# Performance work log

Measured on AMD Instinct MI355X. Metric: run time of the kernel, lower is better.

The kernel has to match this reference:

```python
import jax, jax.numpy as jnp
import numpy as np

N_NODES = 50000
N_EDGES = 1600000
NODE_DIM = 16
EDGE_DIM = 16
PIPE_F = 4
HID = 64
L = 3


def _lin(k, fan_in, fan_out):
    kw, kb = jax.random.split(k)
    bound = 1.0 / np.sqrt(fan_in)
    w = jax.random.uniform(kw, (fan_in, fan_out), jnp.float32, -bound, bound)
    b = jax.random.uniform(kb, (fan_out,), jnp.float32, -bound, bound)
    return w, b


def setup_inputs() -> dict:
    key = jax.random.key(0)
    ks = jax.random.split(key, 16)
    leak_area = jax.random.normal(ks[0], (N_NODES, 1), jnp.float32)
    pipe_attrs = jax.random.normal(ks[1], (N_EDGES, PIPE_F), jnp.float32)
    edge_index = jax.random.randint(ks[2], (2, N_EDGES), 0, N_NODES, jnp.int32)
    node_embed_w, node_embed_b = _lin(ks[3], 1, NODE_DIM)
    edge_embed_w, edge_embed_b = _lin(ks[4], PIPE_F, EDGE_DIM)
    # per-layer MLP params, stacked along leading layer axis
    ew1, eb1, ew2, eb2, nw1, nb1, nw2, nb2 = [], [], [], [], [], [], [], []
    for l in range(L):
        kl = jax.random.fold_in(ks[5], l)
        k1, k2, k3, k4 = jax.random.split(kl, 4)
        w, b = _lin(k1, 2 * NODE_DIM + EDGE_DIM, HID); ew1.append(w); eb1.append(b)
        w, b = _lin(k2, HID, EDGE_DIM); ew2.append(w); eb2.append(b)
        w, b = _lin(k3, NODE_DIM + EDGE_DIM, HID); nw1.append(w); nb1.append(b)
        w, b = _lin(k4, HID, NODE_DIM); nw2.append(w); nb2.append(b)
    final_node_w, final_node_b = _lin(ks[6], NODE_DIM, 1)
    final_edge_w, final_edge_b = _lin(ks[7], EDGE_DIM, 1)
    return {
        "leak_area": leak_area,
        "pipe_attrs": pipe_attrs,
        "edge_index": edge_index,
        "node_embed_w": node_embed_w, "node_embed_b": node_embed_b,
        "edge_embed_w": edge_embed_w, "edge_embed_b": edge_embed_b,
        "edge_mlp_w1": jnp.stack(ew1), "edge_mlp_b1": jnp.stack(eb1),
        "edge_mlp_w2": jnp.stack(ew2), "edge_mlp_b2": jnp.stack(eb2),
        "node_mlp_w1": jnp.stack(nw1), "node_mlp_b1": jnp.stack(nb1),
        "node_mlp_w2": jnp.stack(nw2), "node_mlp_b2": jnp.stack(nb2),
        "final_node_w": final_node_w, "final_node_b": final_node_b,
        "final_edge_w": final_edge_w, "final_edge_b": final_edge_b,
    }


def reference(leak_area, pipe_attrs, edge_index,
              node_embed_w, node_embed_b, edge_embed_w, edge_embed_b,
              edge_mlp_w1, edge_mlp_b1, edge_mlp_w2, edge_mlp_b2,
              node_mlp_w1, node_mlp_b1, node_mlp_w2, node_mlp_b2,
              final_node_w, final_node_b, final_edge_w, final_edge_b):
    x = leak_area @ node_embed_w + node_embed_b          # [N, node_dim]
    e = pipe_attrs @ edge_embed_w + edge_embed_b          # [E, edge_dim]
    src = edge_index[0]  # x_j (source, PyG default flow source_to_target)
    dst = edge_index[1]  # x_i (target); aggregation index
    n = x.shape[0]
    num_layers = edge_mlp_w1.shape[0]
    ones = jnp.ones((src.shape[0], 1), x.dtype)
    deg = jax.ops.segment_sum(ones, dst, num_segments=n)  # [N,1]
    inv_deg = 1.0 / jnp.maximum(deg, 1.0)
    for l in range(num_layers):
        # message: small MLP on [x_i, x_j, e] per edge
        m_in = jnp.concatenate([x[dst], x[src], e], axis=-1)       # [E, 2d+de]
        h = jax.nn.relu(m_in @ edge_mlp_w1[l] + edge_mlp_b1[l])    # [E, 64]
        msg = h @ edge_mlp_w2[l] + edge_mlp_b2[l]                  # [E, de]
        # mean-aggregate to target nodes
        aggr = jax.ops.segment_sum(msg, dst, num_segments=n) * inv_deg  # [N, de]
        # node update MLP
        u_in = jnp.concatenate([x, aggr], axis=-1)                 # [N, d+de]
        x = jax.nn.relu(u_in @ node_mlp_w1[l] + node_mlp_b1[l]) @ node_mlp_w2[l] + node_mlp_b2[l]
    H = (x @ final_node_w + final_node_b)[:, 0]   # [N]
    q = (e @ final_edge_w + final_edge_b)[:, 0]   # [E]
    return H, q
```

## Files before the change

### kernel.cpp

```cpp
#include <hip/hip_runtime.h>
#include <hip/hip_bf16.h>

#define NN 50000
#define NE 1600000
#define NB 391
#define CBLK 392
#define EPB 4096

typedef __attribute__((ext_vector_type(8))) short bf16x8;
typedef __attribute__((ext_vector_type(4))) float f32x4;

#define B_HAG   0
#define B_QW    (B_HAG + NN*64*4)
#define B_NF    (B_QW + 32)
#define B_W1B   (B_NF + 3*8*64*8*2)
#define B_XB0   (B_W1B + 3*8*64*8*2)
#define B_XB1   (B_XB0 + NN*16*2)
#define B_EPK   (B_XB1 + NN*16*2)
#define B_OFF   (B_EPK + NE*16)
#define B_BCNT  (B_OFF + (NN+1)*4)
#define B_BASE  (B_BCNT + CBLK*NB*4)
#define B_GTOT  (B_BASE + (NB+1)*4)
#define B_END   (B_GTOT + NB*4)

static __device__ __forceinline__ unsigned short f2bf(float f) {
    union { __hip_bfloat16 h; unsigned short u; } cv;
    cv.h = __float2bfloat16(f);
    return cv.u;
}
static __device__ __forceinline__ unsigned pk2(float a, float b) {
    unsigned r;
    asm("v_cvt_pk_bf16_f32 %0, %1, %2" : "=v"(r) : "v"(a), "v"(b));
    return r;
}
static __device__ __forceinline__ float bf2f(unsigned short u) {
    return __uint_as_float((unsigned)u << 16);
}
static __device__ __forceinline__ bf16x8 mk8(unsigned a, unsigned b, unsigned c, unsigned d) {
    union { bf16x8 v; uint4 u; } cv;
    cv.u = make_uint4(a, b, c, d);
    return cv.v;
}

__global__ void prep_kernel(const float* __restrict__ ew1, const float* __restrict__ eb1,
                            const float* __restrict__ nw1, const float* __restrict__ ew2,
                            const float* __restrict__ nw2,
                            const float* __restrict__ eeW, const float* __restrict__ eeB,
                            const float* __restrict__ few, const float* __restrict__ feb,
                            unsigned short* __restrict__ w1b, unsigned short* __restrict__ nf,
                            float* __restrict__ qw)
{
    int t0 = blockIdx.x * blockDim.x + threadIdx.x;
    int stride = gridDim.x * blockDim.x;
    for (int idx = t0; idx < 3 * 8 * 64 * 8; idx += stride) {
        int l = idx >> 12;
        int r = idx & 4095;
        int f = r >> 9;
        int lane = (r >> 3) & 63;
        int e = r & 7;
        int col = lane & 15;
        int krow = ((lane >> 4) << 3) + e;
        {
            int tt = f >> 1, s = f & 1;
            int k = krow + (s << 5);
            int j = (tt << 4) + col;
            float v = 0.f;
            if (k < 32) {
                v = ew1[l * 3072 + k * 64 + j];
            } else if (k < 36) {
                int f2 = k - 32;
                float acc = 0.f;
                for (int m = 0; m < 16; m++) acc += eeW[f2 * 16 + m] * ew1[l * 3072 + (32 + m) * 64 + j];
                v = acc;
            } else if (k == 36) {
                float acc = eb1[l * 64 + j];
                for (int m = 0; m < 16; m++) acc += eeB[m] * ew1[l * 3072 + (32 + m) * 64 + j];
                v = acc;
            }
            w1b[idx] = f2bf(v);
        }
        {
            float v;
            if (f < 2)      v = ew2[l * 1024 + (f * 32 + krow) * 16 + col];
            else if (f < 6) v = nw1[l * 2048 + krow * 64 + (f - 2) * 16 + col];
            else            v = nw2[l * 1024 + ((f - 6) * 32 + krow) * 16 + col];
            nf[idx] = f2bf(v);
        }
    }
    if (t0 < 4) {
        float s = 0.f;
        for (int k = 0; k < 16; k++) s += eeW[t0 * 16 + k] * few[k];
        qw[t0] = s;
    } else if (t0 == 4) {
        float s = feb[0];
        for (int k = 0; k < 16; k++) s += eeB[k] * few[k];
        qw[4] = s;
    }
}

__global__ __launch_bounds__(256) void node_init_kernel(
    const float* __restrict__ leak, const float* __restrict__ nw, const float* __restrict__ nb,
    unsigned short* __restrict__ xb0, float* __restrict__ hag)
{
    int n = blockIdx.x * blockDim.x + threadIdx.x;
    if (n >= NN) return;
    float la = leak[n];
    float v[16];
    #pragma unroll
    for (int i = 0; i < 16; i++) v[i] = la * nw[i] + nb[i];
    unsigned pk[8];
    #pragma unroll
    for (int i = 0; i < 8; i++) pk[i] = pk2(v[2 * i], v[2 * i + 1]);
    uint4* xo = reinterpret_cast<uint4*>(xb0 + n * 16);
    xo[0] = make_uint4(pk[0], pk[1], pk[2], pk[3]);
    xo[1] = make_uint4(pk[4], pk[5], pk[6], pk[7]);
    float4 z = {0.f, 0.f, 0.f, 0.f};
    float4* hp = reinterpret_cast<float4*>(hag + n * 64);
    #pragma unroll
    for (int j = 0; j < 16; j++) hp[j] = z;
}

__global__ __launch_bounds__(1024) void bucket_count_kernel(
    const int* __restrict__ dst, int* __restrict__ bcnt)
{
    __shared__ int hist[NB];
    int t = threadIdx.x;
    for (int i = t; i < NB; i += 1024) hist[i] = 0;
    __syncthreads();
    int base = blockIdx.x * EPB;
    int b[4];
    #pragma unroll
    for (int i = 0; i < 4; i++) {
        int idx = base + i * 1024 + t;
        b[i] = (idx < NE) ? (dst[idx] >> 7) : -1;
    }
    #pragma unroll
    for (int i = 0; i < 4; i++)
        if (b[i] >= 0) atomicAdd(&hist[b[i]], 1);
    __syncthreads();
    for (int i = t; i < NB; i += 1024) bcnt[blockIdx.x * NB + i] = hist[i];
}

__global__ __launch_bounds__(512) void scan_blocks_kernel(
    int* __restrict__ bcnt, int* __restrict__ gtot)
{
    __shared__ int sm[512];
    int b = blockIdx.x;
    int t = threadIdx.x;
    int v = (t < CBLK) ? bcnt[t * NB + b] : 0;
    sm[t] = v;
    __syncthreads();
    for (int o = 1; o < 512; o <<= 1) {
        int x = (t >= o) ? sm[t - o] : 0;
        __syncthreads();
        sm[t] += x;
        __syncthreads();
    }
    if (t < CBLK) bcnt[t * NB + b] = sm[t] - v;
    if (t == 511) gtot[b] = sm[511];
}

__global__ __launch_bounds__(512) void scan_top_kernel(
    const int* __restrict__ gtot, int* __restrict__ gbase)
{
    __shared__ int sm[512];
    int t = threadIdx.x;
    int v = (t < NB) ? gtot[t] : 0;
    sm[t] = v;
    __syncthreads();
    for (int o = 1; o < 512; o <<= 1) {
        int x = (t >= o) ? sm[t - o] : 0;
        __syncthreads();
        sm[t] += x;
        __syncthreads();
    }
    if (t < NB) gbase[t] = sm[t] - v;
    if (t == 0) gbase[NB] = NE;
}

__global__ __launch_bounds__(1024) void bucket_scatter_kernel(
    const int* __restrict__ ei, const float* __restrict__ pa,
    const int* __restrict__ bcnt, const int* __restrict__ gbase,
    const float* __restrict__ qw,
    float* __restrict__ qout, uint4* __restrict__ epk)
{
    __shared__ int hist[NB];
    int t = threadIdx.x;
    for (int i = t; i < NB; i += 1024) hist[i] = 0;
    __syncthreads();
    int base = blockIdx.x * EPB;
    float q0 = qw[0], q1 = qw[1], q2 = qw[2], q3 = qw[3], q4 = qw[4];
    int d[4], s[4];
    float4 p[4];
    #pragma unroll
    for (int i = 0; i < 4; i++) {
        int idx = base + i * 1024 + t;
        if (idx < NE) {
            d[i] = ei[NE + idx];
            s[i] = ei[idx];
            p[i] = reinterpret_cast<const float4*>(pa)[idx];
        } else {
            d[i] = -1;
        }
    }
    #pragma unroll
    for (int i = 0; i < 4; i++) {
        int idx = base + i * 1024 + t;
        if (d[i] >= 0)
            qout[idx] = q4 + p[i].x * q0 + p[i].y * q1 + p[i].z * q2 + p[i].w * q3;
    }
    int lr[4];
    #pragma unroll
    for (int i = 0; i < 4; i++)
        if (d[i] >= 0) lr[i] = atomicAdd(&hist[d[i] >> 7], 1);
    int bs[4];
    #pragma unroll
    for (int i = 0; i < 4; i++)
        if (d[i] >= 0) {
            int b = d[i] >> 7;
            bs[i] = gbase[b] + bcnt[blockIdx.x * NB + b];
        }
    #pragma unroll
    for (int i = 0; i < 4; i++)
        if (d[i] >= 0) {
            uint4 v;
            v.x = (unsigned)s[i];
            v.y = (unsigned)d[i];
            v.z = pk2(p[i].x, p[i].y);
            v.w = pk2(p[i].z, p[i].w);
            epk[bs[i] + lr[i]] = v;
        }
}

__global__ __launch_bounds__(1024) void fine_sort_kernel(
    const int* __restrict__ gbase, uint4* __restrict__ epk, int* __restrict__ off)
{
    __shared__ int hist[128];
    __shared__ int fb[128];
    int t = threadIdx.x;
    int b = blockIdx.x;
    int S = gbase[b], E = gbase[b + 1];
    if (t < 128) hist[t] = 0;
    __syncthreads();

    uint4 r[12];
    #pragma unroll
    for (int i = 0; i < 12; i++) {
        int gi = S + i * 1024 + t;
        if (gi < E) r[i] = epk[gi];
    }
    int lr[12];
    #pragma unroll
    for (int i = 0; i < 12; i++) {
        int gi = S + i * 1024 + t;
        if (gi < E) lr[i] = atomicAdd(&hist[(int)(r[i].y & 127u)], 1);
    }
    __syncthreads();
    if (t < 128) fb[t] = hist[t];
    __syncthreads();
    for (int o = 1; o < 128; o <<= 1) {
        int v = 0;
        if (t < 128 && t >= o) v = fb[t - o];
        __syncthreads();
        if (t < 128) fb[t] += v;
        __syncthreads();
    }
    int d0 = b << 7;
    if (t < 128 && d0 + t < NN) off[d0 + t] = S + fb[t] - hist[t];
    if (b == NB - 1 && t == 0) off[NN] = NE;
    __syncthreads();
    #pragma unroll
    for (int i = 0; i < 12; i++) {
        int gi = S + i * 1024 + t;
        if (gi < E) {
            int fd = (int)(r[i].y & 127u);
            int pos = S + (fb[fd] - hist[fd]) + lr[i];
            epk[pos] = r[i];
        }
    }
}

__global__ __launch_bounds__(128, 5) void edge_mfma_kernel(
    const unsigned short* __restrict__ xb,
    const uint4* __restrict__ epk,
    const int* __restrict__ off,
    const unsigned short* __restrict__ w1b,
    float* __restrict__ hag)
{
    __shared__ unsigned short hbuf[2][64 * 68];
    int tid = threadIdx.x;
    int lane = tid & 63;
    int wid = tid >> 6;
    int wave = blockIdx.x * 2 + wid;
    int base = wave * 64;
    if (base >= NE) return;
    int ar = lane & 15;
    int ap = lane >> 4;
    unsigned short* hb = &hbuf[wid][0];

    uint4 ev0 = epk[base + 0  + ar];
    uint4 ev1 = epk[base + 16 + ar];
    uint4 ev2 = epk[base + 32 + ar];
    uint4 ev3 = epk[base + 48 + ar];

    int r0 = (ap < 2) ? (int)ev0.y : (int)ev0.x;
    int r1 = (ap < 2) ? (int)ev1.y : (int)ev1.x;
    int r2 = (ap < 2) ? (int)ev2.y : (int)ev2.x;
    int r3 = (ap < 2) ? (int)ev3.y : (int)ev3.x;
    int half = (ap & 1) * 8;
    bf16x8 a00 = *reinterpret_cast<const bf16x8*>(xb + (size_t)r0 * 16 + half);
    bf16x8 a01 = *reinterpret_cast<const bf16x8*>(xb + (size_t)r1 * 16 + half);
    bf16x8 a02 = *reinterpret_cast<const bf16x8*>(xb + (size_t)r2 * 16 + half);
    bf16x8 a03 = *reinterpret_cast<const bf16x8*>(xb + (size_t)r3 * 16 + half);

    int d0 = __builtin_amdgcn_readfirstlane((int)ev0.y);

    bf16x8 Bf[8];
    const bf16x8* w1v = reinterpret_cast<const bf16x8*>(w1b);
    #pragma unroll
    for (int i = 0; i < 8; i++) Bf[i] = w1v[i * 64 + lane];

#define DO_TILE(EV, A0, TILE) do {                                             \
    bf16x8 a1 = (bf16x8)0;                                                     \
    if (ap == 0) {                                                             \
        a1[0] = (short)(EV.z & 0xffffu);                                       \
        a1[1] = (short)(EV.z >> 16);                                           \
        a1[2] = (short)(EV.w & 0xffffu);                                       \
        a1[3] = (short)(EV.w >> 16);                                           \
        a1[4] = (short)0x3f80;                                                 \
    }                                                                          \
    f32x4 C0 = {0.f, 0.f, 0.f, 0.f}, C1 = C0, C2 = C0, C3 = C0;                \
    C0 = __builtin_amdgcn_mfma_f32_16x16x32_bf16(A0, Bf[0], C0, 0, 0, 0);      \
    C0 = __builtin_amdgcn_mfma_f32_16x16x32_bf16(a1, Bf[1], C0, 0, 0, 0);      \
    C1 = __builtin_amdgcn_mfma_f32_16x16x32_bf16(A0, Bf[2], C1, 0, 0, 0);      \
    C1 = __builtin_amdgcn_mfma_f32_16x16x32_bf16(a1, Bf[3], C1, 0, 0, 0);      \
    C2 = __builtin_amdgcn_mfma_f32_16x16x32_bf16(A0, Bf[4], C2, 0, 0, 0);      \
    C2 = __builtin_amdgcn_mfma_f32_16x16x32_bf16(a1, Bf[5], C2, 0, 0, 0);      \
    C3 = __builtin_amdgcn_mfma_f32_16x16x32_bf16(A0, Bf[6], C3, 0, 0, 0);      \
    C3 = __builtin_amdgcn_mfma_f32_16x16x32_bf16(a1, Bf[7], C3, 0, 0, 0);      \
    int eoff = TILE * 16 + ap * 4;                                             \
    {                                                                          \
        unsigned lov = pk2(fmaxf(C0[0], 0.f), fmaxf(C0[1], 0.f));              \
        unsigned hiv = pk2(fmaxf(C0[2], 0.f), fmaxf(C0[3], 0.f));              \
        *reinterpret_cast<uint2*>(hb + (0 * 16 + ar) * 68 + eoff) = make_uint2(lov, hiv); \
    }                                                                          \
    {                                                                          \
        unsigned lov = pk2(fmaxf(C1[0], 0.f), fmaxf(C1[1], 0.f));              \
        unsigned hiv = pk2(fmaxf(C1[2], 0.f), fmaxf(C1[3], 0.f));              \
        *reinterpret_cast<uint2*>(hb + (1 * 16 + ar) * 68 + eoff) = make_uint2(lov, hiv); \
    }                                                                          \
    {                                                                          \
        unsigned lov = pk2(fmaxf(C2[0], 0.f), fmaxf(C2[1], 0.f));              \
        unsigned hiv = pk2(fmaxf(C2[2], 0.f), fmaxf(C2[3], 0.f));              \
        *reinterpret_cast<uint2*>(hb + (2 * 16 + ar) * 68 + eoff) = make_uint2(lov, hiv); \
    }                                                                          \
    {                                                                          \
        unsigned lov = pk2(fmaxf(C3[0], 0.f), fmaxf(C3[1], 0.f));              \
        unsigned hiv = pk2(fmaxf(C3[2], 0.f), fmaxf(C3[3], 0.f));              \
        *reinterpret_cast<uint2*>(hb + (3 * 16 + ar) * 68 + eoff) = make_uint2(lov, hiv); \
    }                                                                          \
} while (0)

    DO_TILE(ev0, a00, 0);
    DO_TILE(ev1, a01, 1);
    DO_TILE(ev2, a02, 2);
    DO_TILE(ev3, a03, 3);
#undef DO_TILE

    asm volatile("s_waitcnt lgkmcnt(0)" ::: "memory");
    __builtin_amdgcn_sched_barrier(0);

    int d = d0;
    int e = base;
    const int lim = base + 64;
    const unsigned short* hr = hb + lane * 68;
    while (e < lim) {
        int segend = off[d + 1];
        int eend = segend < lim ? segend : lim;
        float acc = 0.f;
        int i = e - base, iend = eend - base;
        for (; (i & 3) != 0 && i < iend; ++i) acc += bf2f(hr[i]);
        for (; i + 4 <= iend; i += 4) {
            uint2 u = *reinterpret_cast<const uint2*>(hr + i);
            acc += __uint_as_float(u.x << 16) + __uint_as_float(u.x & 0xffff0000u)
                 + __uint_as_float(u.y << 16) + __uint_as_float(u.y & 0xffff0000u);
        }
        for (; i < iend; ++i) acc += bf2f(hr[i]);
        unsafeAtomicAdd(&hag[(size_t)d * 64 + lane], acc);
        e = eend;
        if (segend <= lim) ++d;
    }
}

__global__ __launch_bounds__(256) void node_mfma_kernel(
    const unsigned short* __restrict__ xb, unsigned short* __restrict__ xbn,
    float* __restrict__ hag, const int* __restrict__ off,
    const unsigned short* __restrict__ nf,
    const float* __restrict__ eb2,
    const float* __restrict__ nb1, const float* __restrict__ nb2,
    const float* __restrict__ fnw, const float* __restrict__ fnb,
    float* __restrict__ Hout, int writeH)
{
    __shared__ unsigned short aggt[4][16 * 16];
    __shared__ unsigned short ht[4][16 * 64];
    __shared__ float ot[4][16 * 16];
    int tid = threadIdx.x;
    int lane = tid & 63;
    int wid = tid >> 6;
    int wave = blockIdx.x * 4 + wid;
    int n0 = wave * 16;
    if (n0 >= NN) return;
    int nr = lane & 15;
    int ap = lane >> 4;

    bf16x8 Bf[8];
    const bf16x8* nfv = reinterpret_cast<const bf16x8*>(nf);
    #pragma unroll
    for (int i = 0; i < 8; i++) Bf[i] = nfv[i * 64 + lane];

    float* hrow = hag + (size_t)(n0 + nr) * 64 + ap * 8;
    float4* h0p = reinterpret_cast<float4*>(hrow);
    float4* h1p = reinterpret_cast<float4*>(hrow + 32);
    float4 ha = h0p[0], hc = h0p[1];
    float4 he = h1p[0], hg = h1p[1];
    float4 z = {0.f, 0.f, 0.f, 0.f};
    h0p[0] = z; h0p[1] = z; h1p[0] = z; h1p[1] = z;
    bf16x8 agA0 = mk8(pk2(ha.x, ha.y), pk2(ha.z, ha.w), pk2(hc.x, hc.y), pk2(hc.z, hc.w));
    bf16x8 agA1 = mk8(pk2(he.x, he.y), pk2(he.z, he.w), pk2(hg.x, hg.y), pk2(hg.z, hg.w));
    f32x4 Cag = {0.f, 0.f, 0.f, 0.f};
    Cag = __builtin_amdgcn_mfma_f32_16x16x32_bf16(agA0, Bf[0], Cag, 0, 0, 0);
    Cag = __builtin_amdgcn_mfma_f32_16x16x32_bf16(agA1, Bf[1], Cag, 0, 0, 0);

    int bn = n0 + ap * 4;
    int o0 = off[bn], o1 = off[bn + 1], o2 = off[bn + 2], o3 = off[bn + 3], o4 = off[bn + 4];
    float ebv = eb2[nr];
    {
        int dgs[4] = {o1 - o0, o2 - o1, o3 - o2, o4 - o3};
        #pragma unroll
        for (int r = 0; r < 4; r++) {
            float inv = 1.0f / (float)(dgs[r] > 0 ? dgs[r] : 1);
            float val = Cag[r] * inv + ((dgs[r] > 0) ? ebv : 0.f);
            aggt[wid][(ap * 4 + r) * 16 + nr] = f2bf(val);
        }
    }
    asm volatile("s_waitcnt lgkmcnt(0)" ::: "memory");
    __builtin_amdgcn_sched_barrier(0);

    bf16x8 uA;
    if (ap < 2) uA = *reinterpret_cast<const bf16x8*>(xb + (size_t)(n0 + nr) * 16 + ap * 8);
    else        uA = *reinterpret_cast<const bf16x8*>(&aggt[wid][nr * 16 + (ap - 2) * 8]);

    f32x4 Ch0 = {0.f, 0.f, 0.f, 0.f}, Ch1 = Ch0, Ch2 = Ch0, Ch3 = Ch0;
    Ch0 = __builtin_amdgcn_mfma_f32_16x16x32_bf16(uA, Bf[2], Ch0, 0, 0, 0);
    Ch1 = __builtin_amdgcn_mfma_f32_16x16x32_bf16(uA, Bf[3], Ch1, 0, 0, 0);
    Ch2 = __builtin_amdgcn_mfma_f32_16x16x32_bf16(uA, Bf[4], Ch2, 0, 0, 0);
    Ch3 = __builtin_amdgcn_mfma_f32_16x16x32_bf16(uA, Bf[5], Ch3, 0, 0, 0);

#define H_EPI(C, TT) do {                                                      \
    int j = (TT) * 16 + nr;                                                    \
    float bv = nb1[j];                                                         \
    _Pragma("unroll")                                                          \
    for (int r = 0; r < 4; r++) {                                              \
        float h = fmaxf(C[r] + bv, 0.f);                                       \
        ht[wid][(ap * 4 + r) * 64 + j] = f2bf(h);                              \
    }                                                                          \
} while (0)
    H_EPI(Ch0, 0); H_EPI(Ch1, 1); H_EPI(Ch2, 2); H_EPI(Ch3, 3);
#undef H_EPI

    asm volatile("s_waitcnt lgkmcnt(0)" ::: "memory");
    __builtin_amdgcn_sched_barrier(0);

    bf16x8 hA0 = *reinterpret_cast<const bf16x8*>(&ht[wid][nr * 64 + ap * 8]);
    bf16x8 hA1 = *reinterpret_cast<const bf16x8*>(&ht[wid][nr * 64 + 32 + ap * 8]);
    f32x4 Co = {0.f, 0.f, 0.f, 0.f};
    Co = __builtin_amdgcn_mfma_f32_16x16x32_bf16(hA0, Bf[6], Co, 0, 0, 0);
    Co = __builtin_amdgcn_mfma_f32_16x16x32_bf16(hA1, Bf[7], Co, 0, 0, 0);
    {
        float bv = nb2[nr];
        #pragma unroll
        for (int r = 0; r < 4; r++) ot[wid][(ap * 4 + r) * 16 + nr] = Co[r] + bv;
    }
    asm volatile("s_waitcnt lgkmcnt(0)" ::: "memory");
    __builtin_amdgcn_sched_barrier(0);

    if (lane < 16) {
        const float* orow = &ot[wid][lane * 16];
        float o[16];
        #pragma unroll
        for (int k = 0; k < 16; k++) o[k] = orow[k];
        unsigned pk[8];
        #pragma unroll
        for (int i = 0; i < 8; i++) pk[i] = pk2(o[2 * i], o[2 * i + 1]);
        uint4* xo = reinterpret_cast<uint4*>(xbn + (size_t)(n0 + lane) * 16);
        xo[0] = make_uint4(pk[0], pk[1], pk[2], pk[3]);
        xo[1] = make_uint4(pk[4], pk[5], pk[6], pk[7]);
        if (writeH) {
            float s = fnb[0];
            #pragma unroll
            for (int k = 0; k < 16; k++) s += o[k] * fnw[k];
            Hout[n0 + lane] = s;
        }
    }
}

extern "C" void kernel_launch(void* const* d_in, const int* in_sizes, int n_in,
                              void* d_out, int out_size, void* d_ws, size_t ws_size,
                              hipStream_t stream)
{
    const float* leak = (const float*)d_in[0];
    const float* pa   = (const float*)d_in[1];
    const int*   ei   = (const int*)d_in[2];
    const float* neww = (const float*)d_in[3];
    const float* newb = (const float*)d_in[4];
    const float* eeW  = (const float*)d_in[5];
    const float* eeB  = (const float*)d_in[6];
    const float* ew1  = (const float*)d_in[7];
    const float* eb1  = (const float*)d_in[8];
    const float* ew2  = (const float*)d_in[9];
    const float* eb2  = (const float*)d_in[10];
    const float* nw1  = (const float*)d_in[11];
    const float* nb1  = (const float*)d_in[12];
    const float* nw2  = (const float*)d_in[13];
    const float* nb2  = (const float*)d_in[14];
    const float* fnw  = (const float*)d_in[15];
    const float* fnb  = (const float*)d_in[16];
    const float* few  = (const float*)d_in[17];
    const float* feb  = (const float*)d_in[18];

    char* wsb = (char*)d_ws;
    float*          hag   = (float*)(wsb + B_HAG);
    float*          qw    = (float*)(wsb + B_QW);
    unsigned short* nf    = (unsigned short*)(wsb + B_NF);
    unsigned short* w1b   = (unsigned short*)(wsb + B_W1B);
    unsigned short* xb0   = (unsigned short*)(wsb + B_XB0);
    unsigned short* xb1   = (unsigned short*)(wsb + B_XB1);
    uint4*          epk   = (uint4*)(wsb + B_EPK);
    int*            off   = (int*)(wsb + B_OFF);
    int*            bcnt  = (int*)(wsb + B_BCNT);
    int*            gbase = (int*)(wsb + B_BASE);
    int*            gtot  = (int*)(wsb + B_GTOT);

    float* H = (float*)d_out;
    float* q = (float*)d_out + NN;
    const int* dstp = ei + NE;

    prep_kernel<<<16, 256, 0, stream>>>(ew1, eb1, nw1, ew2, nw2, eeW, eeB, few, feb,
                                        w1b, nf, qw);
    node_init_kernel<<<(NN + 255) / 256, 256, 0, stream>>>(leak, neww, newb, xb0, hag);
    bucket_count_kernel<<<CBLK, 1024, 0, stream>>>(dstp, bcnt);
    scan_blocks_kernel<<<NB, 512, 0, stream>>>(bcnt, gtot);
    scan_top_kernel<<<1, 512, 0, stream>>>(gtot, gbase);
    bucket_scatter_kernel<<<CBLK, 1024, 0, stream>>>(ei, pa, bcnt, gbase, qw, q, epk);
    fine_sort_kernel<<<NB, 1024, 0, stream>>>(gbase, epk, off);

    int nwaves = NN / 16;
    int nblocks = (nwaves + 3) / 4;

    unsigned short* xcur = xb0;
    unsigned short* xnxt = xb1;
    for (int l = 0; l < 3; l++) {
        edge_mfma_kernel<<<NE / 128, 128, 0, stream>>>(
            xcur, epk, off, w1b + l * 4096, hag);
        node_mfma_kernel<<<nblocks, 256, 0, stream>>>(
            xcur, xnxt, hag, off, nf + l * 4096, eb2 + l * 16,
            nb1 + l * 64, nb2 + l * 16, fnw, fnb, H, (l == 2) ? 1 : 0);
        unsigned short* tmp = xcur; xcur = xnxt; xnxt = tmp;
    }
}
```

Measured before the change: 198.9 us.

## Store edge hidden activations as fp32 edge-major in LDS with one-wave blocks

The edge kernel now launches one 64-thread wave per block instead of two waves per block. The ReLU'd hidden activations are stored in shared memory as fp32 in an edge-major layout padded to 66 floats per row, replacing the packed bf16 layout transposed per hidden unit. The segment reduction then reads one column per lane with stride 66 and no bf16 unpacking. This removes the bf16 pack/unpack work and a rounding step, but doubles LDS use per wave and replaces vectorised reads with scalar strided reads.

```diff
diff --git a/kernel.cpp b/kernel.cpp
--- a/kernel.cpp
+++ b/kernel.cpp
@@ -32,9 +32,6 @@
     unsigned r;
     asm("v_cvt_pk_bf16_f32 %0, %1, %2" : "=v"(r) : "v"(a), "v"(b));
     return r;
-}
-static __device__ __forceinline__ float bf2f(unsigned short u) {
-    return __uint_as_float((unsigned)u << 16);
 }
 static __device__ __forceinline__ bf16x8 mk8(unsigned a, unsigned b, unsigned c, unsigned d) {
     union { bf16x8 v; uint4 u; } cv;
@@ -280,23 +277,18 @@
     }
 }
 
-__global__ __launch_bounds__(128, 5) void edge_mfma_kernel(
+__global__ __launch_bounds__(64) void edge_mfma_kernel(
     const unsigned short* __restrict__ xb,
     const uint4* __restrict__ epk,
     const int* __restrict__ off,
     const unsigned short* __restrict__ w1b,
     float* __restrict__ hag)
 {
-    __shared__ unsigned short hbuf[2][64 * 68];
-    int tid = threadIdx.x;
-    int lane = tid & 63;
-    int wid = tid >> 6;
-    int wave = blockIdx.x * 2 + wid;
-    int base = wave * 64;
-    if (base >= NE) return;
+    __shared__ float hbf[64 * 66];
+    int lane = threadIdx.x;
+    int base = blockIdx.x * 64;
     int ar = lane & 15;
     int ap = lane >> 4;
-    unsigned short* hb = &hbuf[wid][0];
 
     uint4 ev0 = epk[base + 0  + ar];
     uint4 ev1 = epk[base + 16 + ar];
@@ -319,6 +311,14 @@
     const bf16x8* w1v = reinterpret_cast<const bf16x8*>(w1b);
     #pragma unroll
     for (int i = 0; i < 8; i++) Bf[i] = w1v[i * 64 + lane];
+
+    float* wb = hbf + (ap * 4) * 66 + ar;
+
+#define STORE_Q(C, TILE, Q) do {                                               \
+    _Pragma("unroll")                                                          \
+    for (int r = 0; r < 4; r++)                                                \
+        wb[(size_t)((TILE) * 16 + r) * 66 + (Q) * 16] = fmaxf(C[r], 0.f);      \
+} while (0)
 
 #define DO_TILE(EV, A0, TILE) do {                                             \
     bf16x8 a1 = (bf16x8)0;                                                     \
@@ -338,27 +338,10 @@
     C2 = __builtin_amdgcn_mfma_f32_16x16x32_bf16(a1, Bf[5], C2, 0, 0, 0);      \
     C3 = __builtin_amdgcn_mfma_f32_16x16x32_bf16(A0, Bf[6], C3, 0, 0, 0);      \
     C3 = __builtin_amdgcn_mfma_f32_16x16x32_bf16(a1, Bf[7], C3, 0, 0, 0);      \
-    int eoff = TILE * 16 + ap * 4;                                             \
-    {                                                                          \
-        unsigned lov = pk2(fmaxf(C0[0], 0.f), fmaxf(C0[1], 0.f));              \
-        unsigned hiv = pk2(fmaxf(C0[2], 0.f), fmaxf(C0[3], 0.f));              \
-        *reinterpret_cast<uint2*>(hb + (0 * 16 + ar) * 68 + eoff) = make_uint2(lov, hiv); \
-    }                                                                          \
-    {                                                                          \
-        unsigned lov = pk2(fmaxf(C1[0], 0.f), fmaxf(C1[1], 0.f));              \
-        unsigned hiv = pk2(fmaxf(C1[2], 0.f), fmaxf(C1[3], 0.f));              \
-        *reinterpret_cast<uint2*>(hb + (1 * 16 + ar) * 68 + eoff) = make_uint2(lov, hiv); \
-    }                                                                          \
-    {                                                                          \
-        unsigned lov = pk2(fmaxf(C2[0], 0.f), fmaxf(C2[1], 0.f));              \
-        unsigned hiv = pk2(fmaxf(C2[2], 0.f), fmaxf(C2[3], 0.f));              \
-        *reinterpret_cast<uint2*>(hb + (2 * 16 + ar) * 68 + eoff) = make_uint2(lov, hiv); \
-    }                                                                          \
-    {                                                                          \
-        unsigned lov = pk2(fmaxf(C3[0], 0.f), fmaxf(C3[1], 0.f));              \
-        unsigned hiv = pk2(fmaxf(C3[2], 0.f), fmaxf(C3[3], 0.f));              \
-        *reinterpret_cast<uint2*>(hb + (3 * 16 + ar) * 68 + eoff) = make_uint2(lov, hiv); \
-    }                                                                          \
+    STORE_Q(C0, TILE, 0);                                                      \
+    STORE_Q(C1, TILE, 1);                                                      \
+    STORE_Q(C2, TILE, 2);                                                      \
+    STORE_Q(C3, TILE, 3);                                                      \
 } while (0)
 
     DO_TILE(ev0, a00, 0);
@@ -366,26 +349,25 @@
     DO_TILE(ev2, a02, 2);
     DO_TILE(ev3, a03, 3);
 #undef DO_TILE
+#undef STORE_Q
 
     asm volatile("s_waitcnt lgkmcnt(0)" ::: "memory");
     __builtin_amdgcn_sched_barrier(0);
 
+    const float* col = hbf + lane;
     int d = d0;
     int e = base;
     const int lim = base + 64;
-    const unsigned short* hr = hb + lane * 68;
     while (e < lim) {
         int segend = off[d + 1];
         int eend = segend < lim ? segend : lim;
         float acc = 0.f;
         int i = e - base, iend = eend - base;
-        for (; (i & 3) != 0 && i < iend; ++i) acc += bf2f(hr[i]);
-        for (; i + 4 <= iend; i += 4) {
-            uint2 u = *reinterpret_cast<const uint2*>(hr + i);
-            acc += __uint_as_float(u.x << 16) + __uint_as_float(u.x & 0xffff0000u)
-                 + __uint_as_float(u.y << 16) + __uint_as_float(u.y & 0xffff0000u);
-        }
-        for (; i < iend; ++i) acc += bf2f(hr[i]);
+        for (; i + 2 <= iend; i += 2) {
+            acc += col[(size_t)i * 66];
+            acc += col[(size_t)(i + 1) * 66];
+        }
+        for (; i < iend; ++i) acc += col[(size_t)i * 66];
         unsafeAtomicAdd(&hag[(size_t)d * 64 + lane], acc);
         e = eend;
         if (segend <= lim) ++d;
@@ -560,7 +542,7 @@
     unsigned short* xcur = xb0;
     unsigned short* xnxt = xb1;
     for (int l = 0; l < 3; l++) {
-        edge_mfma_kernel<<<NE / 128, 128, 0, stream>>>(
+        edge_mfma_kernel<<<NE / 64, 64, 0, stream>>>(
             xcur, epk, off, w1b + l * 4096, hag);
         node_mfma_kernel<<<nblocks, 256, 0, stream>>>(
             xcur, xnxt, hag, off, nf + l * 4096, eb2 + l * 16,
```

After: 235.9 us. +18.6%, slower.

## Fuse init kernels and use plain stores for chunk-interior aggregation segments

Applied to the files above, without the earlier changes.

Merges weight prep, node embedding init and the bucket histogram into one launch over the histogram grid, removing two kernel launches and their gaps. Separately, in the edge kernel a destination segment that starts and ends inside the block's 64-edge chunk is written with a plain store instead of an atomic add. This relies on hag being zero beforehand and on no other block touching that row. Boundary segments still use atomics.

```diff
diff --git a/kernel.cpp b/kernel.cpp
--- a/kernel.cpp
+++ b/kernel.cpp
@@ -42,17 +42,37 @@
     return cv.v;
 }
 
-__global__ void prep_kernel(const float* __restrict__ ew1, const float* __restrict__ eb1,
-                            const float* __restrict__ nw1, const float* __restrict__ ew2,
-                            const float* __restrict__ nw2,
-                            const float* __restrict__ eeW, const float* __restrict__ eeB,
-                            const float* __restrict__ few, const float* __restrict__ feb,
-                            unsigned short* __restrict__ w1b, unsigned short* __restrict__ nf,
-                            float* __restrict__ qw)
-{
-    int t0 = blockIdx.x * blockDim.x + threadIdx.x;
-    int stride = gridDim.x * blockDim.x;
-    for (int idx = t0; idx < 3 * 8 * 64 * 8; idx += stride) {
+__global__ __launch_bounds__(1024) void fused_init_kernel(
+    const float* __restrict__ ew1, const float* __restrict__ eb1,
+    const float* __restrict__ nw1, const float* __restrict__ ew2,
+    const float* __restrict__ nw2,
+    const float* __restrict__ eeW, const float* __restrict__ eeB,
+    const float* __restrict__ few, const float* __restrict__ feb,
+    unsigned short* __restrict__ w1b, unsigned short* __restrict__ nf,
+    float* __restrict__ qw,
+    const float* __restrict__ leak, const float* __restrict__ ne_w,
+    const float* __restrict__ ne_b,
+    unsigned short* __restrict__ xb0, float* __restrict__ hag,
+    const int* __restrict__ dst, int* __restrict__ bcnt)
+{
+    __shared__ int hist[NB];
+    int t = threadIdx.x;
+    for (int i = t; i < NB; i += 1024) hist[i] = 0;
+    __syncthreads();
+    int base = blockIdx.x * EPB;
+    int b[4];
+    #pragma unroll
+    for (int i = 0; i < 4; i++) {
+        int idx = base + i * 1024 + t;
+        b[i] = (idx < NE) ? (dst[idx] >> 7) : -1;
+    }
+    #pragma unroll
+    for (int i = 0; i < 4; i++)
+        if (b[i] >= 0) atomicAdd(&hist[b[i]], 1);
+
+    int gtid = blockIdx.x * 1024 + t;
+    int gstride = CBLK * 1024;
+    for (int idx = gtid; idx < 3 * 8 * 64 * 8; idx += gstride) {
         int l = idx >> 12;
         int r = idx & 4095;
         int f = r >> 9;
@@ -87,56 +107,33 @@
             nf[idx] = f2bf(v);
         }
     }
-    if (t0 < 4) {
+    if (gtid < 4) {
         float s = 0.f;
-        for (int k = 0; k < 16; k++) s += eeW[t0 * 16 + k] * few[k];
-        qw[t0] = s;
-    } else if (t0 == 4) {
+        for (int k = 0; k < 16; k++) s += eeW[gtid * 16 + k] * few[k];
+        qw[gtid] = s;
+    } else if (gtid == 4) {
         float s = feb[0];
         for (int k = 0; k < 16; k++) s += eeB[k] * few[k];
         qw[4] = s;
     }
-}
-
-__global__ __launch_bounds__(256) void node_init_kernel(
-    const float* __restrict__ leak, const float* __restrict__ nw, const float* __restrict__ nb,
-    unsigned short* __restrict__ xb0, float* __restrict__ hag)
-{
-    int n = blockIdx.x * blockDim.x + threadIdx.x;
-    if (n >= NN) return;
-    float la = leak[n];
-    float v[16];
-    #pragma unroll
-    for (int i = 0; i < 16; i++) v[i] = la * nw[i] + nb[i];
-    unsigned pk[8];
-    #pragma unroll
-    for (int i = 0; i < 8; i++) pk[i] = pk2(v[2 * i], v[2 * i + 1]);
-    uint4* xo = reinterpret_cast<uint4*>(xb0 + n * 16);
-    xo[0] = make_uint4(pk[0], pk[1], pk[2], pk[3]);
-    xo[1] = make_uint4(pk[4], pk[5], pk[6], pk[7]);
-    float4 z = {0.f, 0.f, 0.f, 0.f};
-    float4* hp = reinterpret_cast<float4*>(hag + n * 64);
-    #pragma unroll
-    for (int j = 0; j < 16; j++) hp[j] = z;
-}
-
-__global__ __launch_bounds__(1024) void bucket_count_kernel(
-    const int* __restrict__ dst, int* __restrict__ bcnt)
-{
-    __shared__ int hist[NB];
-    int t = threadIdx.x;
-    for (int i = t; i < NB; i += 1024) hist[i] = 0;
-    __syncthreads();
-    int base = blockIdx.x * EPB;
-    int b[4];
-    #pragma unroll
-    for (int i = 0; i < 4; i++) {
-        int idx = base + i * 1024 + t;
-        b[i] = (idx < NE) ? (dst[idx] >> 7) : -1;
-    }
-    #pragma unroll
-    for (int i = 0; i < 4; i++)
-        if (b[i] >= 0) atomicAdd(&hist[b[i]], 1);
+    if (gtid < NN) {
+        int n = gtid;
+        float la = leak[n];
+        float v[16];
+        #pragma unroll
+        for (int i = 0; i < 16; i++) v[i] = la * ne_w[i] + ne_b[i];
+        unsigned pk[8];
+        #pragma unroll
+        for (int i = 0; i < 8; i++) pk[i] = pk2(v[2 * i], v[2 * i + 1]);
+        uint4* xo = reinterpret_cast<uint4*>(xb0 + (size_t)n * 16);
+        xo[0] = make_uint4(pk[0], pk[1], pk[2], pk[3]);
+        xo[1] = make_uint4(pk[4], pk[5], pk[6], pk[7]);
+        float4 z = {0.f, 0.f, 0.f, 0.f};
+        float4* hp = reinterpret_cast<float4*>(hag + (size_t)n * 64);
+        #pragma unroll
+        for (int j = 0; j < 16; j++) hp[j] = z;
+    }
+
     __syncthreads();
     for (int i = t; i < NB; i += 1024) bcnt[blockIdx.x * NB + i] = hist[i];
 }
@@ -370,6 +367,7 @@
     asm volatile("s_waitcnt lgkmcnt(0)" ::: "memory");
     __builtin_amdgcn_sched_barrier(0);
 
+    int offd0 = off[d0];
     int d = d0;
     int e = base;
     const int lim = base + 64;
@@ -386,7 +384,11 @@
                  + __uint_as_float(u.y << 16) + __uint_as_float(u.y & 0xffff0000u);
         }
         for (; i < iend; ++i) acc += bf2f(hr[i]);
-        unsafeAtomicAdd(&hag[(size_t)d * 64 + lane], acc);
+        bool interior = (segend <= lim) && (e > base || offd0 == base);
+        if (interior)
+            hag[(size_t)d * 64 + lane] = acc;
+        else
+            unsafeAtomicAdd(&hag[(size_t)d * 64 + lane], acc);
         e = eend;
         if (segend <= lim) ++d;
     }
@@ -545,10 +547,9 @@
     float* q = (float*)d_out + NN;
     const int* dstp = ei + NE;
 
-    prep_kernel<<<16, 256, 0, stream>>>(ew1, eb1, nw1, ew2, nw2, eeW, eeB, few, feb,
-                                        w1b, nf, qw);
-    node_init_kernel<<<(NN + 255) / 256, 256, 0, stream>>>(leak, neww, newb, xb0, hag);
-    bucket_count_kernel<<<CBLK, 1024, 0, stream>>>(dstp, bcnt);
+    fused_init_kernel<<<CBLK, 1024, 0, stream>>>(
+        ew1, eb1, nw1, ew2, nw2, eeW, eeB, few, feb, w1b, nf, qw,
+        leak, neww, newb, xb0, hag, dstp, bcnt);
     scan_blocks_kernel<<<NB, 512, 0, stream>>>(bcnt, gtot);
     scan_top_kernel<<<1, 512, 0, stream>>>(gtot, gbase);
     bucket_scatter_kernel<<<CBLK, 1024, 0, stream>>>(ei, pa, bcnt, gbase, qw, q, epk);
```

Result: no change. 202.2 us (+1.7%).
